# Performance work log

Hardware: AMD Instinct MI355X
Metric: run time of the kernel (lower is better)

The kernel has to match this reference:

```python
import jax, jax.numpy as jnp
import numpy as np

N_NODES = 20000
N_EDGES = 240000
IN_DIM = 20
SH_DIM = 16  # (lmax+1)^2 with lmax=3
DENOM = 1.0
EPS = 1e-12


def spherical_harmonics_lmax3(v):
    """Real spherical harmonics l=0..3 on unit vectors v: [E,3] -> [E,16]."""
    x, y, z = v[:, 0], v[:, 1], v[:, 2]
    x2, y2, z2 = x * x, y * y, z * z
    sh = [
        jnp.full_like(x, 0.28209479177387814),            # l=0
        0.4886025119029199 * y,                            # l=1, m=-1
        0.4886025119029199 * z,                            # l=1, m=0
        0.4886025119029199 * x,                            # l=1, m=1
        1.0925484305920792 * x * y,                        # l=2, m=-2
        1.0925484305920792 * y * z,                        # l=2, m=-1
        0.31539156525252005 * (3.0 * z2 - 1.0),            # l=2, m=0
        1.0925484305920792 * x * z,                        # l=2, m=1
        0.5462742152960396 * (x2 - y2),                    # l=2, m=2
        0.5900435899266435 * y * (3.0 * x2 - y2),          # l=3, m=-3
        2.890611442640554 * x * y * z,                     # l=3, m=-2
        0.4570457994644658 * y * (5.0 * z2 - 1.0),         # l=3, m=-1
        0.3731763325901154 * z * (5.0 * z2 - 3.0),         # l=3, m=0
        0.4570457994644658 * x * (5.0 * z2 - 1.0),         # l=3, m=1
        1.445305721320277 * z * (x2 - y2),                 # l=3, m=2
        0.5900435899266435 * x * (x2 - 3.0 * y2),          # l=3, m=3
    ]
    return jnp.stack(sh, axis=-1)


def setup_inputs() -> dict:
    key = jax.random.key(0)
    ks = jax.random.split(key, 10)
    x = jax.random.normal(ks[0], (N_NODES, IN_DIM), dtype=jnp.float32)
    positions = jax.random.normal(ks[1], (N_NODES, 3), dtype=jnp.float32)
    edge_index = jax.random.randint(ks[2], (2, N_EDGES), 0, N_NODES, dtype=jnp.int32)
    s = 1.0 / np.sqrt(IN_DIM)
    W_pre = jax.random.uniform(ks[3], (IN_DIM, IN_DIM), jnp.float32, -s, s)
    b_pre = jax.random.uniform(ks[4], (IN_DIM,), jnp.float32, -s, s)
    W_post = jax.random.uniform(ks[5], (IN_DIM, IN_DIM), jnp.float32, -s, s)
    b_post = jax.random.uniform(ks[6], (IN_DIM,), jnp.float32, -s, s)
    W_sc = jax.random.uniform(ks[7], (IN_DIM, IN_DIM), jnp.float32, -s, s)
    b_sc = jax.random.uniform(ks[8], (IN_DIM,), jnp.float32, -s, s)
    return {"x": x, "positions": positions, "edge_index": edge_index,
            "W_pre": W_pre, "b_pre": b_pre, "W_post": W_post, "b_post": b_post,
            "W_sc": W_sc, "b_sc": b_sc}


def reference(x, positions, edge_index, W_pre, b_pre, W_post, b_post, W_sc, b_sc):
    row, col = edge_index[0], edge_index[1]
    # per-edge gather + relative positions
    rel = positions[col] - positions[row]                      # [E,3]
    norm = jnp.sqrt(jnp.sum(rel * rel, axis=-1, keepdims=True) + EPS)
    sh = spherical_harmonics_lmax3(rel / norm)                 # [E,16]
    sender = x[row]                                            # [E,20]
    # equivariant tensor product (outer product over irreps channels)
    tp = (sender[:, :, None] * sh[:, None, :]).reshape(sender.shape[0], IN_DIM * SH_DIM)  # [E,320]
    edge_features = jnp.concatenate([sender, tp], axis=1)      # [E,340]
    # scatter-add aggregation to target nodes
    aggr = jax.ops.segment_sum(edge_features, col, num_segments=N_NODES)  # [N,340]
    # node update MLP + shortcut (math of Layer.update)
    h = x / DENOM
    h = jax.nn.relu(h @ W_pre.T + b_pre)
    h = h @ W_post.T + b_post
    out = x @ W_sc.T + b_sc + h                                # [N,20]
    # aggr is computed (and aggregated) by the original propagate; concat so it stays live
    return jnp.concatenate([out, aggr], axis=1)                # [N,360]
```

## Files before the change

### kernel.cpp

```cpp
#include <hip/hip_runtime.h>
#include <stdint.h>

#define N_NODES 20000
#define N_EDGES 240000
#define IN_DIM  20
#define OUT_DIM 360
#define EPS_F   1e-12f
#define NPART   8
#define CAP_P   16
#define SLOTS   (NPART * CAP_P)
#define EDGE_BLOCKS ((N_EDGES + 255) / 256)
#define MLP_BLOCKS  ((N_NODES + 255) / 256)

typedef _Float16 half8   __attribute__((ext_vector_type(8)));
typedef float    floatx16 __attribute__((ext_vector_type(16)));

__device__ __forceinline__ half8 h8_from_u32(uint32_t u0, uint32_t u1,
                                             uint32_t u2, uint32_t u3) {
    union { uint32_t u[4]; half8 h; } t;
    t.u[0] = u0; t.u[1] = u1; t.u[2] = u2; t.u[3] = u3;
    return t.h;
}

__device__ __forceinline__ uint32_t maskpair(int t, int j) {
    return (t > j ? 0xFFFFu : 0u) | (t > j + 1 ? 0xFFFF0000u : 0u);
}

__device__ __forceinline__ float sh_coeff(int k, float xn, float yn, float zn) {
    const float x2 = xn * xn, y2 = yn * yn, z2 = zn * zn;
    switch (k) {
        case 0:  return 0.28209479177387814f;
        case 1:  return 0.4886025119029199f * yn;
        case 2:  return 0.4886025119029199f * zn;
        case 3:  return 0.4886025119029199f * xn;
        case 4:  return 1.0925484305920792f * xn * yn;
        case 5:  return 1.0925484305920792f * yn * zn;
        case 6:  return 0.31539156525252005f * (3.0f * z2 - 1.0f);
        case 7:  return 1.0925484305920792f * xn * zn;
        case 8:  return 0.5462742152960396f * (x2 - y2);
        case 9:  return 0.5900435899266435f * yn * (3.0f * x2 - y2);
        case 10: return 2.890611442640554f  * xn * yn * zn;
        case 11: return 0.4570457994644658f * yn * (5.0f * z2 - 1.0f);
        case 12: return 0.3731763325901154f * zn * (5.0f * z2 - 3.0f);
        case 13: return 0.4570457994644658f * xn * (5.0f * z2 - 1.0f);
        case 14: return 1.445305721320277f  * zn * (x2 - y2);
        default: return 0.5900435899266435f * xn * (x2 - 3.0f * y2);
    }
}

__global__ __launch_bounds__(256) void bucket_mlp(
    const int* __restrict__ ei,
    const float* __restrict__ x,
    const float* __restrict__ Wpre,  const float* __restrict__ bpre,
    const float* __restrict__ Wpost, const float* __restrict__ bpost,
    const float* __restrict__ Wsc,   const float* __restrict__ bsc,
    int* __restrict__ cnt_pad,
    int* __restrict__ ovf_cnt,
    int* __restrict__ ovf,
    int* __restrict__ bucket,
    uint32_t* __restrict__ xpair,
    float* __restrict__ out)
{
    if ((int)blockIdx.x < EDGE_BLOCKS) {
        const int e = (int)(blockIdx.x * 256 + threadIdx.x);
        if (e >= N_EDGES) return;
        const int p = (int)(blockIdx.x & (NPART - 1));
        const int row = ei[e];
        const int col = ei[N_EDGES + e];
        const int slot = atomicAdd(&cnt_pad[((size_t)(p * N_NODES + col)) << 4], 1);
        if (slot >= CAP_P) { ovf[atomicAdd(ovf_cnt, 1)] = e; return; }
        bucket[col * SLOTS + (p << 4) + slot] = row;
        return;
    }

    __shared__ float sWpre[IN_DIM * IN_DIM];
    __shared__ float sWpost[IN_DIM * IN_DIM];
    __shared__ float sWsc[IN_DIM * IN_DIM];
    __shared__ float sb[3 * IN_DIM];

    for (int t = threadIdx.x; t < IN_DIM * IN_DIM; t += 256) {
        sWpre[t]  = Wpre[t];
        sWpost[t] = Wpost[t];
        sWsc[t]   = Wsc[t];
    }
    if (threadIdx.x < IN_DIM) {
        sb[threadIdx.x]              = bpre[threadIdx.x];
        sb[IN_DIM + threadIdx.x]     = bpost[threadIdx.x];
        sb[2 * IN_DIM + threadIdx.x] = bsc[threadIdx.x];
    }
    __syncthreads();

    const int i = (int)((blockIdx.x - EDGE_BLOCKS) * 256 + threadIdx.x);
    if (i >= N_NODES) return;

    float xi[IN_DIM], h[IN_DIM];
#pragma unroll
    for (int j = 0; j < IN_DIM; ++j) xi[j] = x[(size_t)i * IN_DIM + j];

#pragma unroll
    for (int j = 0; j < IN_DIM; ++j) {
        const float v = xi[j];
        const _Float16 hh = (_Float16)v;
        const float res = v - (float)hh;
        union { _Float16 f[2]; uint32_t u; } t;
        t.f[0] = hh; t.f[1] = (_Float16)res;
        xpair[(size_t)i * IN_DIM + j] = t.u;
    }

#pragma unroll
    for (int j = 0; j < IN_DIM; ++j) {
        float a = sb[j];
#pragma unroll
        for (int kk = 0; kk < IN_DIM; ++kk) a = fmaf(xi[kk], sWpre[j * IN_DIM + kk], a);
        h[j] = fmaxf(a, 0.0f);
    }
#pragma unroll
    for (int j = 0; j < IN_DIM; ++j) {
        float a = sb[IN_DIM + j] + sb[2 * IN_DIM + j];
#pragma unroll
        for (int kk = 0; kk < IN_DIM; ++kk) {
            a = fmaf(h[kk],  sWpost[j * IN_DIM + kk], a);
            a = fmaf(xi[kk], sWsc[j * IN_DIM + kk],  a);
        }
        out[(size_t)i * OUT_DIM + j] = a;
    }
}

__global__ __launch_bounds__(256) void node_gather(
    const float* __restrict__ x,
    const float* __restrict__ pos,
    const int* __restrict__ ei,
    const int* __restrict__ cnt_pad,
    const int* __restrict__ bucket,
    const uint32_t* __restrict__ xpair,
    const int* __restrict__ ovf_cnt,
    const int* __restrict__ ovf,
    float* __restrict__ out)
{
    __shared__ uint16_t shls[4][64][16];

    const int lane  = threadIdx.x & 63;
    const int w     = (int)(threadIdx.x >> 6);
    const int node  = __builtin_amdgcn_readfirstlane(
        (int)((blockIdx.x * blockDim.x + threadIdx.x) >> 6));
    const int col   = lane & 31;
    const int hi    = lane >> 5;
    const int khalf = hi * 8;
    const int rowc  = min(col, IN_DIM - 1);

    int ovf_any = 0;
    int c[NPART];
#pragma unroll
    for (int q = 0; q < NPART; ++q) {
        const int cr = __builtin_amdgcn_readfirstlane(
            cnt_pad[((size_t)(q * N_NODES + node)) << 4]);
        ovf_any |= (cr > CAP_P);
        c[q] = min(cr, CAP_P);
    }
    int pre = 0, pp = 0, base = 0;
#pragma unroll
    for (int q = 0; q < NPART; ++q) {
        if (q >= 1) {
            const int ge = (lane >= pre) ? 1 : 0;
            pp  += ge;
            base = ge ? pre : base;
        }
        pre += c[q];
    }
    const int cnt = min(pre, 64);
    const int s  = min(lane - base, CAP_P - 1);
    const int m  = (pp << 4) + s;

    const int rl = (int)min((uint32_t)bucket[node * SLOTS + m],
                            (uint32_t)(N_NODES - 1));

    {
        const float pnx = pos[node * 3 + 0];
        const float pny = pos[node * 3 + 1];
        const float pnz = pos[node * 3 + 2];
        const float rx = pnx - pos[rl * 3 + 0];
        const float ry = pny - pos[rl * 3 + 1];
        const float rz = pnz - pos[rl * 3 + 2];
        const float rinv = rsqrtf(rx * rx + ry * ry + rz * rz + EPS_F);
        const float xx = rx * rinv, yy = ry * rinv, zz = rz * rinv;
        const float x2 = xx * xx, y2 = yy * yy, z2 = zz * zz;

        const float sh0  = 0.28209479177387814f;
        const float sh1  = 0.4886025119029199f * yy;
        const float sh2  = 0.4886025119029199f * zz;
        const float sh3  = 0.4886025119029199f * xx;
        const float sh4  = 1.0925484305920792f * xx * yy;
        const float sh5  = 1.0925484305920792f * yy * zz;
        const float sh6  = 0.31539156525252005f * (3.0f * z2 - 1.0f);
        const float sh7  = 1.0925484305920792f * xx * zz;
        const float sh8  = 0.5462742152960396f * (x2 - y2);
        const float sh9  = 0.5900435899266435f * yy * (3.0f * x2 - y2);
        const float sh10 = 2.890611442640554f  * xx * yy * zz;
        const float sh11 = 0.4570457994644658f * yy * (5.0f * z2 - 1.0f);
        const float sh12 = 0.3731763325901154f * zz * (5.0f * z2 - 3.0f);
        const float sh13 = 0.4570457994644658f * xx * (5.0f * z2 - 1.0f);
        const float sh14 = 1.445305721320277f  * zz * (x2 - y2);
        const float sh15 = 0.5900435899266435f * xx * (x2 - 3.0f * y2);

        const half8 v0 = { (_Float16)sh0,  (_Float16)sh1,  (_Float16)sh2,  (_Float16)sh3,
                           (_Float16)sh4,  (_Float16)sh5,  (_Float16)sh6,  (_Float16)sh7 };
        const half8 v1 = { (_Float16)sh8,  (_Float16)sh9,  (_Float16)sh10, (_Float16)sh11,
                           (_Float16)sh12, (_Float16)sh13, (_Float16)sh14, (_Float16)sh15 };
        half8* wp = (half8*)&shls[w][lane][0];
        wp[0] = v0;
        wp[1] = v1;
    }
    __syncthreads();

    floatx16 acc = {0,0,0,0,0,0,0,0,0,0,0,0,0,0,0,0};

    if (cnt > 0) {
        const int nb = (cnt + 15) >> 4;

        for (int b = 0; b < nb; ++b) {
            const int sbase = 16 * b + khalf;

            int rr[8];
#pragma unroll
            for (int j = 0; j < 8; ++j)
                rr[j] = __shfl(rl, sbase + j, 64);
            uint32_t ee[8];
#pragma unroll
            for (int j = 0; j < 8; ++j)
                ee[j] = xpair[(size_t)rr[j] * IN_DIM + rowc];

            uint32_t B0, B1, B2, B3;
            if (col < 16) {
                const uint32_t h0 = shls[w][sbase + 0][col];
                const uint32_t h1 = shls[w][sbase + 1][col];
                const uint32_t h2 = shls[w][sbase + 2][col];
                const uint32_t h3 = shls[w][sbase + 3][col];
                const uint32_t h4 = shls[w][sbase + 4][col];
                const uint32_t h5 = shls[w][sbase + 5][col];
                const uint32_t h6 = shls[w][sbase + 6][col];
                const uint32_t h7 = shls[w][sbase + 7][col];
                B0 = h0 | (h1 << 16);
                B1 = h2 | (h3 << 16);
                B2 = h4 | (h5 << 16);
                B3 = h6 | (h7 << 16);
            } else if (col == 16) {
                B0 = B1 = B2 = B3 = 0x3C003C00u;
            } else {
                B0 = B1 = B2 = B3 = 0u;
            }
            const int rem = cnt - 16 * b;
            if (rem < 16) {
                const int t = rem - khalf;
                B0 &= maskpair(t, 0);
                B1 &= maskpair(t, 2);
                B2 &= maskpair(t, 4);
                B3 &= maskpair(t, 6);
            }

            uint32_t a1u[4], a2u[4];
#pragma unroll
            for (int pq = 0; pq < 4; ++pq) {
                a1u[pq] = (ee[2 * pq] & 0xFFFFu)  | (ee[2 * pq + 1] << 16);
                a2u[pq] = (ee[2 * pq] >> 16)      | (ee[2 * pq + 1] & 0xFFFF0000u);
            }

            const half8 hb  = h8_from_u32(B0, B1, B2, B3);
            const half8 ha1 = h8_from_u32(a1u[0], a1u[1], a1u[2], a1u[3]);
            const half8 ha2 = h8_from_u32(a2u[0], a2u[1], a2u[2], a2u[3]);
            acc = __builtin_amdgcn_mfma_f32_32x32x16_f16(ha1, hb, acc, 0, 0, 0);
            acc = __builtin_amdgcn_mfma_f32_32x32x16_f16(ha2, hb, acc, 0, 0, 0);
        }
    }

    if (ovf_any) {
        const int mm = *ovf_cnt;
        for (int t2 = 0; t2 < mm; ++t2) {
            const int e = ovf[t2];
            if (ei[N_EDGES + e] != node) continue;
            const int row = ei[e];
            const float rx = pos[node * 3 + 0] - pos[row * 3 + 0];
            const float ry = pos[node * 3 + 1] - pos[row * 3 + 1];
            const float rz = pos[node * 3 + 2] - pos[row * 3 + 2];
            const float rinv = rsqrtf(rx * rx + ry * ry + rz * rz + EPS_F);
            float shc;
            if (col < 16)       shc = sh_coeff(col, rx * rinv, ry * rinv, rz * rinv);
            else if (col == 16) shc = 1.0f;
            else                shc = 0.0f;
#pragma unroll
            for (int r = 0; r < 16; ++r) {
                const int rw = ((r & 3) + 8 * (r >> 2)) + 4 * hi;
                if (rw < IN_DIM)
                    acc[r] = fmaf(x[(size_t)row * IN_DIM + rw], shc, acc[r]);
            }
        }
    }

    float* orow = out + (size_t)node * OUT_DIM;
    if (col < 16) {
#pragma unroll
        for (int r = 0; r < 16; ++r) {
            const int rw = ((r & 3) + 8 * (r >> 2)) + 4 * hi;
            if (rw < IN_DIM) orow[2 * IN_DIM + rw * 16 + col] = acc[r];
        }
    } else if (col == 16) {
#pragma unroll
        for (int r = 0; r < 16; ++r) {
            const int rw = ((r & 3) + 8 * (r >> 2)) + 4 * hi;
            if (rw < IN_DIM) orow[IN_DIM + rw] = acc[r];
        }
    }
}

extern "C" void kernel_launch(void* const* d_in, const int* in_sizes, int n_in,
                              void* d_out, int out_size, void* d_ws, size_t ws_size,
                              hipStream_t stream)
{
    const float* x     = (const float*)d_in[0];
    const float* pos   = (const float*)d_in[1];
    const int*   ei    = (const int*)d_in[2];
    const float* Wpre  = (const float*)d_in[3];
    const float* bpre  = (const float*)d_in[4];
    const float* Wpost = (const float*)d_in[5];
    const float* bpost = (const float*)d_in[6];
    const float* Wsc   = (const float*)d_in[7];
    const float* bsc   = (const float*)d_in[8];
    float* out = (float*)d_out;

    char* wp = (char*)d_ws;
    int*      bucket  = (int*)wp;                 wp += (size_t)N_NODES * SLOTS * 4;
    uint32_t* xpair   = (uint32_t*)wp;            wp += (size_t)N_NODES * IN_DIM * 4;
    int*      cnt_pad = (int*)wp;                 wp += (size_t)NPART * N_NODES * 64;
    int*      ovf_cnt = (int*)wp;                 wp += 4;
    int*      ovf     = (int*)wp;

    hipMemsetAsync(cnt_pad, 0, (size_t)NPART * N_NODES * 64 + 4, stream);

    bucket_mlp<<<EDGE_BLOCKS + MLP_BLOCKS, 256, 0, stream>>>(
        ei, x, Wpre, bpre, Wpost, bpost, Wsc, bsc,
        cnt_pad, ovf_cnt, ovf, bucket, xpair, out);

    node_gather<<<(N_NODES * 64) / 256, 256, 0, stream>>>(
        x, pos, ei, cnt_pad, bucket, xpair, ovf_cnt, ovf, out);
}
```

Baseline: 116.6 us.

## Replace atomic partitioned bucketing with LDS histogram counting sort

Edge bucketing by target node now uses a counting sort: per-block LDS histograms with per-edge ranks, a per-node prefix scan fused into the MLP kernel, then an atomic-free scatter into contiguous 64-slot buckets. This removes the memset and the global atomics on padded counters, and simplifies the slot-index computation in the gather kernel. It adds two kernel launches and several MB of histogram and base-offset traffic, and the histogram kernel uses only 64 blocks.

```diff
diff --git a/kernel.cpp b/kernel.cpp
--- a/kernel.cpp
+++ b/kernel.cpp
@@ -6,9 +6,10 @@
 #define IN_DIM  20
 #define OUT_DIM 360
 #define EPS_F   1e-12f
-#define NPART   8
-#define CAP_P   16
-#define SLOTS   (NPART * CAP_P)
+#define CAP     64
+#define NB      64
+#define EPB     (N_EDGES / NB)
+#define HALF    (N_NODES / 2)
 #define EDGE_BLOCKS ((N_EDGES + 255) / 256)
 #define MLP_BLOCKS  ((N_NODES + 255) / 256)
 
@@ -48,37 +49,49 @@
     }
 }
 
-__global__ __launch_bounds__(256) void bucket_mlp(
+__global__ __launch_bounds__(1024) void edge_hist(
     const int* __restrict__ ei,
+    uint32_t* __restrict__ ghist,
+    uint16_t* __restrict__ rank)
+{
+    __shared__ uint32_t lh[HALF];
+    const int b  = (int)blockIdx.x;
+    const int e0 = b * EPB;
+
+    for (int p = 0; p < 2; ++p) {
+        for (int t = (int)threadIdx.x; t < HALF; t += 1024) lh[t] = 0;
+        __syncthreads();
+        for (int t = (int)threadIdx.x; t < EPB; t += 1024) {
+            const int e = e0 + t;
+            const int c = ei[N_EDGES + e] - p * HALF;
+            if (c >= 0 && c < HALF)
+                rank[e] = (uint16_t)atomicAdd(&lh[c], 1u);
+        }
+        __syncthreads();
+        for (int t = (int)threadIdx.x; t < HALF; t += 1024)
+            ghist[(size_t)b * N_NODES + p * HALF + t] = lh[t];
+        __syncthreads();
+    }
+}
+
+__global__ __launch_bounds__(256) void scan_mlp(
     const float* __restrict__ x,
     const float* __restrict__ Wpre,  const float* __restrict__ bpre,
     const float* __restrict__ Wpost, const float* __restrict__ bpost,
     const float* __restrict__ Wsc,   const float* __restrict__ bsc,
-    int* __restrict__ cnt_pad,
+    const uint32_t* __restrict__ ghist,
+    uint32_t* __restrict__ gbase,
+    int* __restrict__ counts,
     int* __restrict__ ovf_cnt,
-    int* __restrict__ ovf,
-    int* __restrict__ bucket,
     uint32_t* __restrict__ xpair,
     float* __restrict__ out)
 {
-    if ((int)blockIdx.x < EDGE_BLOCKS) {
-        const int e = (int)(blockIdx.x * 256 + threadIdx.x);
-        if (e >= N_EDGES) return;
-        const int p = (int)(blockIdx.x & (NPART - 1));
-        const int row = ei[e];
-        const int col = ei[N_EDGES + e];
-        const int slot = atomicAdd(&cnt_pad[((size_t)(p * N_NODES + col)) << 4], 1);
-        if (slot >= CAP_P) { ovf[atomicAdd(ovf_cnt, 1)] = e; return; }
-        bucket[col * SLOTS + (p << 4) + slot] = row;
-        return;
-    }
-
     __shared__ float sWpre[IN_DIM * IN_DIM];
     __shared__ float sWpost[IN_DIM * IN_DIM];
     __shared__ float sWsc[IN_DIM * IN_DIM];
     __shared__ float sb[3 * IN_DIM];
 
-    for (int t = threadIdx.x; t < IN_DIM * IN_DIM; t += 256) {
+    for (int t = (int)threadIdx.x; t < IN_DIM * IN_DIM; t += 256) {
         sWpre[t]  = Wpre[t];
         sWpost[t] = Wpost[t];
         sWsc[t]   = Wsc[t];
@@ -90,12 +103,22 @@
     }
     __syncthreads();
 
-    const int i = (int)((blockIdx.x - EDGE_BLOCKS) * 256 + threadIdx.x);
-    if (i >= N_NODES) return;
+    const int n = (int)(blockIdx.x * 256 + threadIdx.x);
+    if (blockIdx.x == 0 && threadIdx.x == 0) *ovf_cnt = 0;
+    if (n >= N_NODES) return;
+
+    uint32_t s = 0;
+#pragma unroll 4
+    for (int b = 0; b < NB; ++b) {
+        const uint32_t v = ghist[(size_t)b * N_NODES + n];
+        gbase[(size_t)b * N_NODES + n] = s;
+        s += v;
+    }
+    counts[n] = (int)s;
 
     float xi[IN_DIM], h[IN_DIM];
 #pragma unroll
-    for (int j = 0; j < IN_DIM; ++j) xi[j] = x[(size_t)i * IN_DIM + j];
+    for (int j = 0; j < IN_DIM; ++j) xi[j] = x[(size_t)n * IN_DIM + j];
 
 #pragma unroll
     for (int j = 0; j < IN_DIM; ++j) {
@@ -104,7 +127,7 @@
         const float res = v - (float)hh;
         union { _Float16 f[2]; uint32_t u; } t;
         t.f[0] = hh; t.f[1] = (_Float16)res;
-        xpair[(size_t)i * IN_DIM + j] = t.u;
+        xpair[(size_t)n * IN_DIM + j] = t.u;
     }
 
 #pragma unroll
@@ -122,15 +145,33 @@
             a = fmaf(h[kk],  sWpost[j * IN_DIM + kk], a);
             a = fmaf(xi[kk], sWsc[j * IN_DIM + kk],  a);
         }
-        out[(size_t)i * OUT_DIM + j] = a;
-    }
+        out[(size_t)n * OUT_DIM + j] = a;
+    }
+}
+
+__global__ __launch_bounds__(256) void scatter(
+    const int* __restrict__ ei,
+    const uint32_t* __restrict__ gbase,
+    const uint16_t* __restrict__ rank,
+    int* __restrict__ ovf_cnt,
+    int* __restrict__ ovf,
+    int* __restrict__ bucket)
+{
+    const int e = (int)(blockIdx.x * 256 + threadIdx.x);
+    if (e >= N_EDGES) return;
+    const int row = ei[e];
+    const int col = ei[N_EDGES + e];
+    const int b   = e / EPB;
+    const int slot = (int)(gbase[(size_t)b * N_NODES + col] + (uint32_t)rank[e]);
+    if (slot >= CAP) { ovf[atomicAdd(ovf_cnt, 1)] = e; return; }
+    bucket[col * CAP + slot] = row;
 }
 
 __global__ __launch_bounds__(256) void node_gather(
     const float* __restrict__ x,
     const float* __restrict__ pos,
     const int* __restrict__ ei,
-    const int* __restrict__ cnt_pad,
+    const int* __restrict__ counts,
     const int* __restrict__ bucket,
     const uint32_t* __restrict__ xpair,
     const int* __restrict__ ovf_cnt,
@@ -148,30 +189,10 @@
     const int khalf = hi * 8;
     const int rowc  = min(col, IN_DIM - 1);
 
-    int ovf_any = 0;
-    int c[NPART];
-#pragma unroll
-    for (int q = 0; q < NPART; ++q) {
-        const int cr = __builtin_amdgcn_readfirstlane(
-            cnt_pad[((size_t)(q * N_NODES + node)) << 4]);
-        ovf_any |= (cr > CAP_P);
-        c[q] = min(cr, CAP_P);
-    }
-    int pre = 0, pp = 0, base = 0;
-#pragma unroll
-    for (int q = 0; q < NPART; ++q) {
-        if (q >= 1) {
-            const int ge = (lane >= pre) ? 1 : 0;
-            pp  += ge;
-            base = ge ? pre : base;
-        }
-        pre += c[q];
-    }
-    const int cnt = min(pre, 64);
-    const int s  = min(lane - base, CAP_P - 1);
-    const int m  = (pp << 4) + s;
-
-    const int rl = (int)min((uint32_t)bucket[node * SLOTS + m],
+    const int cnt_raw = __builtin_amdgcn_readfirstlane(counts[node]);
+    const int cnt = min(cnt_raw, CAP);
+
+    const int rl = (int)min((uint32_t)bucket[node * CAP + lane],
                             (uint32_t)(N_NODES - 1));
 
     {
@@ -272,7 +293,7 @@
         }
     }
 
-    if (ovf_any) {
+    if (cnt_raw > CAP) {
         const int mm = *ovf_cnt;
         for (int t2 = 0; t2 < mm; ++t2) {
             const int e = ovf[t2];
@@ -327,18 +348,23 @@
     float* out = (float*)d_out;
 
     char* wp = (char*)d_ws;
-    int*      bucket  = (int*)wp;                 wp += (size_t)N_NODES * SLOTS * 4;
-    uint32_t* xpair   = (uint32_t*)wp;            wp += (size_t)N_NODES * IN_DIM * 4;
-    int*      cnt_pad = (int*)wp;                 wp += (size_t)NPART * N_NODES * 64;
-    int*      ovf_cnt = (int*)wp;                 wp += 4;
+    int*      bucket  = (int*)wp;        wp += (size_t)N_NODES * CAP * 4;
+    uint32_t* xpair   = (uint32_t*)wp;   wp += (size_t)N_NODES * IN_DIM * 4;
+    uint32_t* ghist   = (uint32_t*)wp;   wp += (size_t)NB * N_NODES * 4;
+    uint32_t* gbase   = (uint32_t*)wp;   wp += (size_t)NB * N_NODES * 4;
+    uint16_t* rank    = (uint16_t*)wp;   wp += (size_t)N_EDGES * 2;
+    int*      counts  = (int*)wp;        wp += (size_t)N_NODES * 4;
+    int*      ovf_cnt = (int*)wp;        wp += 4;
     int*      ovf     = (int*)wp;
 
-    hipMemsetAsync(cnt_pad, 0, (size_t)NPART * N_NODES * 64 + 4, stream);
-
-    bucket_mlp<<<EDGE_BLOCKS + MLP_BLOCKS, 256, 0, stream>>>(
-        ei, x, Wpre, bpre, Wpost, bpost, Wsc, bsc,
-        cnt_pad, ovf_cnt, ovf, bucket, xpair, out);
+    edge_hist<<<NB, 1024, 0, stream>>>(ei, ghist, rank);
+
+    scan_mlp<<<MLP_BLOCKS, 256, 0, stream>>>(
+        x, Wpre, bpre, Wpost, bpost, Wsc, bsc,
+        ghist, gbase, counts, ovf_cnt, xpair, out);
+
+    scatter<<<EDGE_BLOCKS, 256, 0, stream>>>(ei, gbase, rank, ovf_cnt, ovf, bucket);
 
     node_gather<<<(N_NODES * 64) / 256, 256, 0, stream>>>(
-        x, pos, ei, cnt_pad, bucket, xpair, ovf_cnt, ovf, out);
-}
+        x, pos, ei, counts, bucket, xpair, ovf_cnt, ovf, out);
+}
```

Result: slower. 121.4 us (+4.1%).
